# Performance work log

Hardware: AMD Instinct MI355X
Metric: run time of the kernel (lower is better)

The kernel has to match this reference:

```python
import jax, jax.numpy as jnp
import numpy as np
import math

N = 128
SIZE = N * N
K = 16
ORDER = 2
DIM = 2

def _exponents(order):
    # 2D Taylor monomial exponents (a,b) with 1 <= a+b <= order
    return [(a, d - a) for d in range(1, order + 1) for a in range(d, -1, -1)]

EXPS = _exponents(ORDER)
NUM_DERIV = len(EXPS)  # n(n+3)/2 = 5 for order 2, matches TP_layer.num_derivatives


def setup_inputs() -> dict:
    key = jax.random.key(0)
    k0, k1, k2, k3, k4 = jax.random.split(key, 5)
    B = 32
    x = jax.random.normal(k0, (B, SIZE), dtype=jnp.float32)
    points = jax.random.uniform(k1, (B, SIZE, DIM), dtype=jnp.float32)
    edge_index = jax.random.randint(k2, (B, SIZE * K), 0, SIZE)
    dist = jax.random.uniform(k3, (B, SIZE, K), dtype=jnp.float32)
    dt = jnp.float32(0.01)
    # PDELinear weight: shape (1, 1, num_derivatives), uniform(-0.1, 0.1)
    weight = jax.random.uniform(k4, (1, 1, NUM_DERIV), dtype=jnp.float32,
                                minval=-0.1, maxval=0.1)
    return {"x": x, "points": points, "edge_index": edge_index,
            "dt": dt, "dist": dist, "weight": weight}


def _solve_derivatives(points, knn_points, values, knn_values, dist):
    # points: [B,S,2]  knn_points: [B,S,K,2]  values: [B,S]  knn_values: [B,S,K]
    off = knn_points - points[:, :, None, :]          # [B,S,K,2]
    dx, dy = off[..., 0], off[..., 1]
    cols = [(dx ** a) * (dy ** b) / (math.factorial(a) * math.factorial(b))
            for (a, b) in EXPS]
    A = jnp.stack(cols, axis=-1)                      # [B,S,K,D] Taylor design matrix
    rhs = knn_values - values[..., None]              # [B,S,K]
    Aw = A * dist[..., None]                          # weighted least squares
    bw = rhs * dist
    AtA = jnp.einsum('bski,bskj->bsij', Aw, Aw)       # [B,S,D,D]
    Atb = jnp.einsum('bski,bsk->bsi', Aw, bw)         # [B,S,D]
    ridge = jnp.float32(1e-6) * jnp.eye(NUM_DERIV, dtype=A.dtype)
    deriv = jnp.linalg.solve(AtA + ridge, Atb[..., None])[..., 0]  # [B,S,D]
    return deriv


def reference(x, points, edge_index, dt, dist, weight):
    B = x.shape[0]
    values = x.reshape(B, SIZE)
    # per-batch kNN gather (vectorized index_select)
    knn_p = jnp.take_along_axis(points, edge_index[..., None], axis=1)
    knn_p = knn_p.reshape(B, SIZE, K, DIM)
    knn_v = jnp.take_along_axis(values[..., None], edge_index[..., None], axis=1)
    knn_v = knn_v.reshape(B, SIZE, K)
    deriv = _solve_derivatives(points, knn_p, values, knn_v, dist)
    deriv = jax.lax.stop_gradient(deriv)              # torch.no_grad in original
    du = jnp.sum(deriv * weight[0], axis=-1)          # PDELinear broadcast + sum -> [B,S]
    return x + dt * du
```

## Files before the change

kernel.cpp:

```cpp
#include <hip/hip_runtime.h>

#define TPL_SIZE 16384
#define TPL_K 16
#define TPL_ND 5
#define TPL_BLK 512
#define TPL_PTS 4
#define TPL_SPAN (TPL_BLK * TPL_PTS)
#define TPL_BPB (TPL_SIZE / TPL_SPAN)
#define TPL_NXCD 8

typedef __attribute__((ext_vector_type(2))) float f32x2;

__global__ __launch_bounds__(TPL_BLK, 2) void tp_lds_kernel(
    const float* __restrict__ x,
    const float* __restrict__ points,
    const int*   __restrict__ edge_index,
    const float* __restrict__ dtp,
    const float* __restrict__ dist,
    const float* __restrict__ weight,
    float* __restrict__ out)
{
    extern __shared__ uint2 lds_pv[];

    const int tid = threadIdx.x;
    const int blk = blockIdx.x;

    const int xcd   = blk & (TPL_NXCD - 1);
    const int batch = xcd * 4 + (blk >> 6);
    const int chunk = (blk >> 3) & (TPL_BPB - 1);

    const size_t base = (size_t)batch * TPL_SIZE + chunk * TPL_SPAN;

    int4   ci[4];
    float4 cw[4];
    {
        const int4*   ei = reinterpret_cast<const int4*>(edge_index + (base + tid) * TPL_K);
        const float4* dw = reinterpret_cast<const float4*>(dist      + (base + tid) * TPL_K);
        ci[0] = ei[0]; ci[1] = ei[1]; ci[2] = ei[2]; ci[3] = ei[3];
        cw[0] = dw[0]; cw[1] = dw[1]; cw[2] = dw[2]; cw[3] = dw[3];
    }

    {
        const float4* pb4 = reinterpret_cast<const float4*>(points + (size_t)batch * TPL_SIZE * 2);
        const float2* xb2 = reinterpret_cast<const float2*>(x + (size_t)batch * TPL_SIZE);
        uint4* lds4 = reinterpret_cast<uint4*>(lds_pv);
        #pragma unroll
        for (int k = 0; k < TPL_SIZE / (2 * TPL_BLK); ++k) {
            int g = k * TPL_BLK + tid;
            float4 pp = pb4[g];
            float2 xv = xb2[g];
            unsigned ux0 = (unsigned)(pp.x * 65536.0f);
            unsigned uy0 = (unsigned)(pp.y * 65536.0f);
            unsigned ux1 = (unsigned)(pp.z * 65536.0f);
            unsigned uy1 = (unsigned)(pp.w * 65536.0f);
            if (ux0 > 65535u) ux0 = 65535u;
            if (uy0 > 65535u) uy0 = 65535u;
            if (ux1 > 65535u) ux1 = 65535u;
            if (uy1 > 65535u) uy1 = 65535u;
            uint4 wv;
            wv.x = ux0 | (uy0 << 16);
            wv.y = __float_as_uint(xv.x);
            wv.z = ux1 | (uy1 << 16);
            wv.w = __float_as_uint(xv.y);
            lds4[g] = wv;
        }
    }
    __syncthreads();

    const float wt0 = weight[0], wt1 = weight[1], wt2 = weight[2],
                wt3 = weight[3], wt4 = weight[4];
    const float dtv = dtp[0];

    #pragma unroll
    for (int p = 0; p < TPL_PTS; ++p) {
        int4   ni[4];
        float4 nw[4];
        if (p < TPL_PTS - 1) {
            const size_t rown = base + (p + 1) * TPL_BLK + tid;
            const int4*   ei = reinterpret_cast<const int4*>(edge_index + rown * TPL_K);
            const float4* dw = reinterpret_cast<const float4*>(dist      + rown * TPL_K);
            ni[0] = ei[0]; ni[1] = ei[1]; ni[2] = ei[2]; ni[3] = ei[3];
            nw[0] = dw[0]; nw[1] = dw[1]; nw[2] = dw[2]; nw[3] = dw[3];
        }

        const int    s   = chunk * TPL_SPAN + p * TPL_BLK + tid;
        const size_t row = base + p * TPL_BLK + tid;

        uint2 se = lds_pv[s];
        unsigned sx = se.x & 0xffffu;
        unsigned sy = se.x >> 16;
        float    sv = __uint_as_float(se.y);

        int ids[TPL_K] = {ci[0].x, ci[0].y, ci[0].z, ci[0].w,
                          ci[1].x, ci[1].y, ci[1].z, ci[1].w,
                          ci[2].x, ci[2].y, ci[2].z, ci[2].w,
                          ci[3].x, ci[3].y, ci[3].z, ci[3].w};
        float wgt[TPL_K] = {cw[0].x, cw[0].y, cw[0].z, cw[0].w,
                            cw[1].x, cw[1].y, cw[1].z, cw[1].w,
                            cw[2].x, cw[2].y, cw[2].z, cw[2].w,
                            cw[3].x, cw[3].y, cw[3].z, cw[3].w};

        uint2 nb[TPL_K];
        #pragma unroll
        for (int t = 0; t < TPL_K; ++t) nb[t] = lds_pv[ids[t] & (TPL_SIZE - 1)];

        f32x2 ata2[15], atb2[TPL_ND];
        #pragma unroll
        for (int i = 0; i < 15; ++i) ata2[i] = (f32x2)0.0f;
        #pragma unroll
        for (int i = 0; i < TPL_ND; ++i) atb2[i] = (f32x2)0.0f;

        #pragma unroll
        for (int tt = 0; tt < TPL_K / 2; ++tt) {
            const int t0 = 2 * tt, t1 = 2 * tt + 1;
            int dxi0 = (int)(nb[t0].x & 0xffffu) - (int)sx;
            int dyi0 = (int)(nb[t0].x >> 16)     - (int)sy;
            int dxi1 = (int)(nb[t1].x & 0xffffu) - (int)sx;
            int dyi1 = (int)(nb[t1].x >> 16)     - (int)sy;
            f32x2 dx = (f32x2){(float)dxi0, (float)dxi1} * 0x1p-16f;
            f32x2 dy = (f32x2){(float)dyi0, (float)dyi1} * 0x1p-16f;
            f32x2 w  = {wgt[t0], wgt[t1]};
            f32x2 nv = {__uint_as_float(nb[t0].y), __uint_as_float(nb[t1].y)};
            f32x2 hw = w * 0.5f;
            f32x2 a[TPL_ND];
            a[0] = dx * w;
            a[1] = dy * w;
            a[2] = dx * dx * hw;
            a[3] = dx * dy * w;
            a[4] = dy * dy * hw;
            f32x2 bwv = (nv - sv) * w;
            int c = 0;
            #pragma unroll
            for (int i = 0; i < TPL_ND; ++i) {
                #pragma unroll
                for (int j = i; j < TPL_ND; ++j) { ata2[c] += a[i] * a[j]; ++c; }
                atb2[i] += a[i] * bwv;
            }
        }

        float ata[15], atb[TPL_ND];
        #pragma unroll
        for (int i = 0; i < 15; ++i) ata[i] = ata2[i].x + ata2[i].y;
        #pragma unroll
        for (int i = 0; i < TPL_ND; ++i) atb[i] = atb2[i].x + atb2[i].y;

        float M[TPL_ND][TPL_ND], r[TPL_ND], pinv[TPL_ND];
        {
            int c = 0;
            #pragma unroll
            for (int i = 0; i < TPL_ND; ++i) {
                #pragma unroll
                for (int j = i; j < TPL_ND; ++j) { M[i][j] = ata[c]; M[j][i] = ata[c]; ++c; }
                r[i] = atb[i];
                M[i][i] += 1e-6f;
            }
        }
        #pragma unroll
        for (int i = 0; i < TPL_ND; ++i) {
            float inv = __builtin_amdgcn_rcpf(M[i][i]);
            pinv[i] = inv;
            #pragma unroll
            for (int j = i + 1; j < TPL_ND; ++j) {
                float f = M[j][i] * inv;
                #pragma unroll
                for (int cc = i + 1; cc < TPL_ND; ++cc) M[j][cc] -= f * M[i][cc];
                r[j] -= f * r[i];
            }
        }
        float sol[TPL_ND];
        #pragma unroll
        for (int i = TPL_ND - 1; i >= 0; --i) {
            float sv2 = r[i];
            #pragma unroll
            for (int cc = i + 1; cc < TPL_ND; ++cc) sv2 -= M[i][cc] * sol[cc];
            sol[i] = sv2 * pinv[i];
        }

        float du = sol[0] * wt0 + sol[1] * wt1 + sol[2] * wt2
                 + sol[3] * wt3 + sol[4] * wt4;
        out[row] = sv + dtv * du;

        if (p < TPL_PTS - 1) {
            #pragma unroll
            for (int q = 0; q < 4; ++q) { ci[q] = ni[q]; cw[q] = nw[q]; }
        }
    }
}

extern "C" void kernel_launch(void* const* d_in, const int* in_sizes, int n_in,
                              void* d_out, int out_size, void* d_ws, size_t ws_size,
                              hipStream_t stream) {
    const float* x          = (const float*)d_in[0];
    const float* points     = (const float*)d_in[1];
    const int*   edge_index = (const int*)d_in[2];
    const float* dtp        = (const float*)d_in[3];
    const float* dist       = (const float*)d_in[4];
    const float* weight     = (const float*)d_in[5];
    float* out = (float*)d_out;

    int total = out_size;
    int grid  = total / TPL_SPAN;
    size_t lds_bytes = (size_t)TPL_SIZE * sizeof(uint2);

    tp_lds_kernel<<<grid, TPL_BLK, lds_bytes, stream>>>(
        x, points, edge_index, dtp, dist, weight, out);
}
```

Measured before the change: 21.04 us.

## Process two points per thread in packed f32x2 lanes including the solve

Each thread now handles two points at a time (A and B) packed into the two lanes of f32x2 vectors. Accumulation, Gaussian elimination and back-substitution all run on packed math, so the scalar 5x5 solve is vectorized. Previously only the 16-neighbor accumulation was split across lanes, followed by a horizontal reduction. Prefetching now loads the next pair's indices and weights, which doubles register pressure for the index and weight buffers and risks lower occupancy at 512 threads with 2 blocks.

```diff
diff --git a/kernel.cpp b/kernel.cpp
--- a/kernel.cpp
+++ b/kernel.cpp
@@ -5,6 +5,7 @@
 #define TPL_ND 5
 #define TPL_BLK 512
 #define TPL_PTS 4
+#define TPL_PAIRS (TPL_PTS / 2)
 #define TPL_SPAN (TPL_BLK * TPL_PTS)
 #define TPL_BPB (TPL_SIZE / TPL_SPAN)
 #define TPL_NXCD 8
@@ -31,13 +32,18 @@
 
     const size_t base = (size_t)batch * TPL_SIZE + chunk * TPL_SPAN;
 
-    int4   ci[4];
-    float4 cw[4];
+    int4   ciA[4], ciB[4];
+    float4 cwA[4], cwB[4];
     {
-        const int4*   ei = reinterpret_cast<const int4*>(edge_index + (base + tid) * TPL_K);
-        const float4* dw = reinterpret_cast<const float4*>(dist      + (base + tid) * TPL_K);
-        ci[0] = ei[0]; ci[1] = ei[1]; ci[2] = ei[2]; ci[3] = ei[3];
-        cw[0] = dw[0]; cw[1] = dw[1]; cw[2] = dw[2]; cw[3] = dw[3];
+        const int4*   eA = reinterpret_cast<const int4*>(edge_index + (base + tid) * TPL_K);
+        const float4* dA = reinterpret_cast<const float4*>(dist      + (base + tid) * TPL_K);
+        const int4*   eB = reinterpret_cast<const int4*>(edge_index + (base + TPL_BLK + tid) * TPL_K);
+        const float4* dB = reinterpret_cast<const float4*>(dist      + (base + TPL_BLK + tid) * TPL_K);
+        #pragma unroll
+        for (int q = 0; q < 4; ++q) {
+            ciA[q] = eA[q]; cwA[q] = dA[q];
+            ciB[q] = eB[q]; cwB[q] = dB[q];
+        }
     }
 
     {
@@ -72,37 +78,54 @@
     const float dtv = dtp[0];
 
     #pragma unroll
-    for (int p = 0; p < TPL_PTS; ++p) {
-        int4   ni[4];
-        float4 nw[4];
-        if (p < TPL_PTS - 1) {
-            const size_t rown = base + (p + 1) * TPL_BLK + tid;
-            const int4*   ei = reinterpret_cast<const int4*>(edge_index + rown * TPL_K);
-            const float4* dw = reinterpret_cast<const float4*>(dist      + rown * TPL_K);
-            ni[0] = ei[0]; ni[1] = ei[1]; ni[2] = ei[2]; ni[3] = ei[3];
-            nw[0] = dw[0]; nw[1] = dw[1]; nw[2] = dw[2]; nw[3] = dw[3];
-        }
-
-        const int    s   = chunk * TPL_SPAN + p * TPL_BLK + tid;
-        const size_t row = base + p * TPL_BLK + tid;
-
-        uint2 se = lds_pv[s];
-        unsigned sx = se.x & 0xffffu;
-        unsigned sy = se.x >> 16;
-        float    sv = __uint_as_float(se.y);
-
-        int ids[TPL_K] = {ci[0].x, ci[0].y, ci[0].z, ci[0].w,
-                          ci[1].x, ci[1].y, ci[1].z, ci[1].w,
-                          ci[2].x, ci[2].y, ci[2].z, ci[2].w,
-                          ci[3].x, ci[3].y, ci[3].z, ci[3].w};
-        float wgt[TPL_K] = {cw[0].x, cw[0].y, cw[0].z, cw[0].w,
-                            cw[1].x, cw[1].y, cw[1].z, cw[1].w,
-                            cw[2].x, cw[2].y, cw[2].z, cw[2].w,
-                            cw[3].x, cw[3].y, cw[3].z, cw[3].w};
-
-        uint2 nb[TPL_K];
-        #pragma unroll
-        for (int t = 0; t < TPL_K; ++t) nb[t] = lds_pv[ids[t] & (TPL_SIZE - 1)];
+    for (int pp = 0; pp < TPL_PAIRS; ++pp) {
+        const int    sA   = chunk * TPL_SPAN + (2 * pp) * TPL_BLK + tid;
+        const int    sB   = sA + TPL_BLK;
+        const size_t rowA = base + (2 * pp) * TPL_BLK + tid;
+        const size_t rowB = rowA + TPL_BLK;
+
+        uint2 seA = lds_pv[sA];
+        uint2 seB = lds_pv[sB];
+        const int sxA = (int)(seA.x & 0xffffu), syA = (int)(seA.x >> 16);
+        const int sxB = (int)(seB.x & 0xffffu), syB = (int)(seB.x >> 16);
+        const f32x2 sv2 = {__uint_as_float(seA.y), __uint_as_float(seB.y)};
+
+        int   idsA[TPL_K], idsB[TPL_K];
+        f32x2 wgt2[TPL_K];
+        #pragma unroll
+        for (int q = 0; q < 4; ++q) {
+            idsA[4*q+0] = ciA[q].x; idsA[4*q+1] = ciA[q].y;
+            idsA[4*q+2] = ciA[q].z; idsA[4*q+3] = ciA[q].w;
+            idsB[4*q+0] = ciB[q].x; idsB[4*q+1] = ciB[q].y;
+            idsB[4*q+2] = ciB[q].z; idsB[4*q+3] = ciB[q].w;
+            wgt2[4*q+0] = (f32x2){cwA[q].x, cwB[q].x};
+            wgt2[4*q+1] = (f32x2){cwA[q].y, cwB[q].y};
+            wgt2[4*q+2] = (f32x2){cwA[q].z, cwB[q].z};
+            wgt2[4*q+3] = (f32x2){cwA[q].w, cwB[q].w};
+        }
+
+        uint2 nA[TPL_K], nB[TPL_K];
+        #pragma unroll
+        for (int t = 0; t < TPL_K; ++t) {
+            nA[t] = lds_pv[idsA[t] & (TPL_SIZE - 1)];
+            nB[t] = lds_pv[idsB[t] & (TPL_SIZE - 1)];
+        }
+
+        int4   niA[4], niB[4];
+        float4 nwA[4], nwB[4];
+        if (pp + 1 < TPL_PAIRS) {
+            const size_t rA = base + (2 * (pp + 1)) * TPL_BLK + tid;
+            const size_t rB = rA + TPL_BLK;
+            const int4*   eA = reinterpret_cast<const int4*>(edge_index + rA * TPL_K);
+            const float4* dA = reinterpret_cast<const float4*>(dist      + rA * TPL_K);
+            const int4*   eB = reinterpret_cast<const int4*>(edge_index + rB * TPL_K);
+            const float4* dB = reinterpret_cast<const float4*>(dist      + rB * TPL_K);
+            #pragma unroll
+            for (int q = 0; q < 4; ++q) {
+                niA[q] = eA[q]; nwA[q] = dA[q];
+                niB[q] = eB[q]; nwB[q] = dB[q];
+            }
+        }
 
         f32x2 ata2[15], atb2[TPL_ND];
         #pragma unroll
@@ -111,16 +134,15 @@
         for (int i = 0; i < TPL_ND; ++i) atb2[i] = (f32x2)0.0f;
 
         #pragma unroll
-        for (int tt = 0; tt < TPL_K / 2; ++tt) {
-            const int t0 = 2 * tt, t1 = 2 * tt + 1;
-            int dxi0 = (int)(nb[t0].x & 0xffffu) - (int)sx;
-            int dyi0 = (int)(nb[t0].x >> 16)     - (int)sy;
-            int dxi1 = (int)(nb[t1].x & 0xffffu) - (int)sx;
-            int dyi1 = (int)(nb[t1].x >> 16)     - (int)sy;
-            f32x2 dx = (f32x2){(float)dxi0, (float)dxi1} * 0x1p-16f;
-            f32x2 dy = (f32x2){(float)dyi0, (float)dyi1} * 0x1p-16f;
-            f32x2 w  = {wgt[t0], wgt[t1]};
-            f32x2 nv = {__uint_as_float(nb[t0].y), __uint_as_float(nb[t1].y)};
+        for (int t = 0; t < TPL_K; ++t) {
+            int dxiA = (int)(nA[t].x & 0xffffu) - sxA;
+            int dyiA = (int)(nA[t].x >> 16)     - syA;
+            int dxiB = (int)(nB[t].x & 0xffffu) - sxB;
+            int dyiB = (int)(nB[t].x >> 16)     - syB;
+            f32x2 dx = (f32x2){(float)dxiA, (float)dxiB} * 0x1p-16f;
+            f32x2 dy = (f32x2){(float)dyiA, (float)dyiB} * 0x1p-16f;
+            f32x2 w  = wgt2[t];
+            f32x2 nv = {__uint_as_float(nA[t].y), __uint_as_float(nB[t].y)};
             f32x2 hw = w * 0.5f;
             f32x2 a[TPL_ND];
             a[0] = dx * w;
@@ -128,7 +150,7 @@
             a[2] = dx * dx * hw;
             a[3] = dx * dy * w;
             a[4] = dy * dy * hw;
-            f32x2 bwv = (nv - sv) * w;
+            f32x2 bwv = (nv - sv2) * w;
             int c = 0;
             #pragma unroll
             for (int i = 0; i < TPL_ND; ++i) {
@@ -138,51 +160,50 @@
             }
         }
 
-        float ata[15], atb[TPL_ND];
-        #pragma unroll
-        for (int i = 0; i < 15; ++i) ata[i] = ata2[i].x + ata2[i].y;
-        #pragma unroll
-        for (int i = 0; i < TPL_ND; ++i) atb[i] = atb2[i].x + atb2[i].y;
-
-        float M[TPL_ND][TPL_ND], r[TPL_ND], pinv[TPL_ND];
+        f32x2 M2[TPL_ND][TPL_ND], r2[TPL_ND], pinv2[TPL_ND];
         {
             int c = 0;
             #pragma unroll
             for (int i = 0; i < TPL_ND; ++i) {
                 #pragma unroll
-                for (int j = i; j < TPL_ND; ++j) { M[i][j] = ata[c]; M[j][i] = ata[c]; ++c; }
-                r[i] = atb[i];
-                M[i][i] += 1e-6f;
+                for (int j = i; j < TPL_ND; ++j) { M2[i][j] = ata2[c]; M2[j][i] = ata2[c]; ++c; }
+                r2[i] = atb2[i];
+                M2[i][i] += 1e-6f;
             }
         }
         #pragma unroll
         for (int i = 0; i < TPL_ND; ++i) {
-            float inv = __builtin_amdgcn_rcpf(M[i][i]);
-            pinv[i] = inv;
+            f32x2 inv2 = {__builtin_amdgcn_rcpf(M2[i][i].x),
+                          __builtin_amdgcn_rcpf(M2[i][i].y)};
+            pinv2[i] = inv2;
             #pragma unroll
             for (int j = i + 1; j < TPL_ND; ++j) {
-                float f = M[j][i] * inv;
+                f32x2 f = M2[j][i] * inv2;
                 #pragma unroll
-                for (int cc = i + 1; cc < TPL_ND; ++cc) M[j][cc] -= f * M[i][cc];
-                r[j] -= f * r[i];
-            }
-        }
-        float sol[TPL_ND];
+                for (int cc = i + 1; cc < TPL_ND; ++cc) M2[j][cc] -= f * M2[i][cc];
+                r2[j] -= f * r2[i];
+            }
+        }
+        f32x2 sol2[TPL_ND];
         #pragma unroll
         for (int i = TPL_ND - 1; i >= 0; --i) {
-            float sv2 = r[i];
-            #pragma unroll
-            for (int cc = i + 1; cc < TPL_ND; ++cc) sv2 -= M[i][cc] * sol[cc];
-            sol[i] = sv2 * pinv[i];
-        }
-
-        float du = sol[0] * wt0 + sol[1] * wt1 + sol[2] * wt2
-                 + sol[3] * wt3 + sol[4] * wt4;
-        out[row] = sv + dtv * du;
-
-        if (p < TPL_PTS - 1) {
-            #pragma unroll
-            for (int q = 0; q < 4; ++q) { ci[q] = ni[q]; cw[q] = nw[q]; }
+            f32x2 acc = r2[i];
+            #pragma unroll
+            for (int cc = i + 1; cc < TPL_ND; ++cc) acc -= M2[i][cc] * sol2[cc];
+            sol2[i] = acc * pinv2[i];
+        }
+
+        f32x2 du2 = sol2[0] * wt0 + sol2[1] * wt1 + sol2[2] * wt2
+                  + sol2[3] * wt3 + sol2[4] * wt4;
+        out[rowA] = sv2.x + dtv * du2.x;
+        out[rowB] = sv2.y + dtv * du2.y;
+
+        if (pp + 1 < TPL_PAIRS) {
+            #pragma unroll
+            for (int q = 0; q < 4; ++q) {
+                ciA[q] = niA[q]; cwA[q] = nwA[q];
+                ciB[q] = niB[q]; cwB[q] = nwB[q];
+            }
         }
     }
 }
```

After: 21.67 us. +3.0%, slower.

## Pre-pack point/value table in separate kernel and bulk-load it into LDS

Applied to the files above, without the earlier changes.

Adds a pack kernel that quantizes points and interleaves them with x into a uint2 table in workspace. The main kernel then fills LDS with direct global-to-LDS loads instead of having each block repeat the conversion. The next row's index/weight prefetch moves to after the neighbor gathers, and the index mask is dropped. The cost is an extra launch plus a table write and read round-trip. Blocks of the same batch no longer redo the packing work, though they still each load the full table.

```diff
diff --git a/kernel.cpp b/kernel.cpp
--- a/kernel.cpp
+++ b/kernel.cpp
@@ -11,7 +11,182 @@
 
 typedef __attribute__((ext_vector_type(2))) float f32x2;
 
+__global__ __launch_bounds__(256) void tp_pack_kernel(
+    const float* __restrict__ x,
+    const float* __restrict__ points,
+    uint2* __restrict__ table,
+    int total)
+{
+    int gid = blockIdx.x * blockDim.x + threadIdx.x;
+    if (gid >= total) return;
+    float2 p = reinterpret_cast<const float2*>(points)[gid];
+    float  v = x[gid];
+    unsigned ux = (unsigned)(p.x * 65536.0f);
+    unsigned uy = (unsigned)(p.y * 65536.0f);
+    if (ux > 65535u) ux = 65535u;
+    if (uy > 65535u) uy = 65535u;
+    uint2 e;
+    e.x = ux | (uy << 16);
+    e.y = __float_as_uint(v);
+    table[gid] = e;
+}
+
 __global__ __launch_bounds__(TPL_BLK, 2) void tp_lds_kernel(
+    const uint2* __restrict__ table,
+    const int*   __restrict__ edge_index,
+    const float* __restrict__ dtp,
+    const float* __restrict__ dist,
+    const float* __restrict__ weight,
+    float* __restrict__ out)
+{
+    extern __shared__ uint2 lds_pv[];
+
+    const int tid = threadIdx.x;
+    const int blk = blockIdx.x;
+
+    const int xcd   = blk & (TPL_NXCD - 1);
+    const int batch = xcd * 4 + (blk >> 6);
+    const int chunk = (blk >> 3) & (TPL_BPB - 1);
+
+    const size_t base = (size_t)batch * TPL_SIZE + chunk * TPL_SPAN;
+
+    int4   ci[4];
+    float4 cw[4];
+    {
+        const int4*   ei = reinterpret_cast<const int4*>(edge_index + (base + tid) * TPL_K);
+        const float4* dw = reinterpret_cast<const float4*>(dist      + (base + tid) * TPL_K);
+        ci[0] = ei[0]; ci[1] = ei[1]; ci[2] = ei[2]; ci[3] = ei[3];
+        cw[0] = dw[0]; cw[1] = dw[1]; cw[2] = dw[2]; cw[3] = dw[3];
+    }
+
+    {
+        const uint32_t* tb = reinterpret_cast<const uint32_t*>(table + (size_t)batch * TPL_SIZE);
+        uint32_t* lraw = reinterpret_cast<uint32_t*>(lds_pv);
+        #pragma unroll
+        for (int k = 0; k < (TPL_SIZE * 8) / (TPL_BLK * 16); ++k) {
+            int i = k * TPL_BLK + tid;
+            __builtin_amdgcn_global_load_lds(
+                (const __attribute__((address_space(1))) uint32_t*)(tb) + (size_t)i * 4,
+                (__attribute__((address_space(3))) uint32_t*)(lraw) + (size_t)i * 4,
+                16, 0, 0);
+        }
+    }
+    __syncthreads();
+
+    const float wt0 = weight[0], wt1 = weight[1], wt2 = weight[2],
+                wt3 = weight[3], wt4 = weight[4];
+    const float dtv = dtp[0];
+
+    #pragma unroll
+    for (int p = 0; p < TPL_PTS; ++p) {
+        const int    s   = chunk * TPL_SPAN + p * TPL_BLK + tid;
+        const size_t row = base + p * TPL_BLK + tid;
+
+        uint2 se = lds_pv[s];
+        const int sx = (int)(se.x & 0xffffu);
+        const int sy = (int)(se.x >> 16);
+        const float sv = __uint_as_float(se.y);
+
+        int ids[TPL_K] = {ci[0].x, ci[0].y, ci[0].z, ci[0].w,
+                          ci[1].x, ci[1].y, ci[1].z, ci[1].w,
+                          ci[2].x, ci[2].y, ci[2].z, ci[2].w,
+                          ci[3].x, ci[3].y, ci[3].z, ci[3].w};
+        float wgt[TPL_K] = {cw[0].x, cw[0].y, cw[0].z, cw[0].w,
+                            cw[1].x, cw[1].y, cw[1].z, cw[1].w,
+                            cw[2].x, cw[2].y, cw[2].z, cw[2].w,
+                            cw[3].x, cw[3].y, cw[3].z, cw[3].w};
+
+        uint2 nb[TPL_K];
+        #pragma unroll
+        for (int t = 0; t < TPL_K; ++t) nb[t] = lds_pv[ids[t]];
+
+        if (p < TPL_PTS - 1) {
+            const size_t rown = base + (p + 1) * TPL_BLK + tid;
+            const int4*   ei = reinterpret_cast<const int4*>(edge_index + rown * TPL_K);
+            const float4* dw = reinterpret_cast<const float4*>(dist      + rown * TPL_K);
+            #pragma unroll
+            for (int q = 0; q < 4; ++q) { ci[q] = ei[q]; cw[q] = dw[q]; }
+        }
+
+        f32x2 ata2[15], atb2[TPL_ND];
+        #pragma unroll
+        for (int i = 0; i < 15; ++i) ata2[i] = (f32x2)0.0f;
+        #pragma unroll
+        for (int i = 0; i < TPL_ND; ++i) atb2[i] = (f32x2)0.0f;
+
+        #pragma unroll
+        for (int tt = 0; tt < TPL_K / 2; ++tt) {
+            const int t0 = 2 * tt, t1 = 2 * tt + 1;
+            int dxi0 = (int)(nb[t0].x & 0xffffu) - sx;
+            int dyi0 = (int)(nb[t0].x >> 16)     - sy;
+            int dxi1 = (int)(nb[t1].x & 0xffffu) - sx;
+            int dyi1 = (int)(nb[t1].x >> 16)     - sy;
+            f32x2 dx = (f32x2){(float)dxi0, (float)dxi1} * 0x1p-16f;
+            f32x2 dy = (f32x2){(float)dyi0, (float)dyi1} * 0x1p-16f;
+            f32x2 w  = {wgt[t0], wgt[t1]};
+            f32x2 nv = {__uint_as_float(nb[t0].y), __uint_as_float(nb[t1].y)};
+            f32x2 hw = w * 0.5f;
+            f32x2 a[TPL_ND];
+            a[0] = dx * w;
+            a[1] = dy * w;
+            a[2] = dx * dx * hw;
+            a[3] = dx * dy * w;
+            a[4] = dy * dy * hw;
+            f32x2 bwv = (nv - sv) * w;
+            int c = 0;
+            #pragma unroll
+            for (int i = 0; i < TPL_ND; ++i) {
+                #pragma unroll
+                for (int j = i; j < TPL_ND; ++j) { ata2[c] += a[i] * a[j]; ++c; }
+                atb2[i] += a[i] * bwv;
+            }
+        }
+
+        float ata[15], atb[TPL_ND];
+        #pragma unroll
+        for (int i = 0; i < 15; ++i) ata[i] = ata2[i].x + ata2[i].y;
+        #pragma unroll
+        for (int i = 0; i < TPL_ND; ++i) atb[i] = atb2[i].x + atb2[i].y;
+
+        float M[TPL_ND][TPL_ND], r[TPL_ND], pinv[TPL_ND];
+        {
+            int c = 0;
+            #pragma unroll
+            for (int i = 0; i < TPL_ND; ++i) {
+                #pragma unroll
+                for (int j = i; j < TPL_ND; ++j) { M[i][j] = ata[c]; M[j][i] = ata[c]; ++c; }
+                r[i] = atb[i];
+                M[i][i] += 1e-6f;
+            }
+        }
+        #pragma unroll
+        for (int i = 0; i < TPL_ND; ++i) {
+            float inv = __builtin_amdgcn_rcpf(M[i][i]);
+            pinv[i] = inv;
+            #pragma unroll
+            for (int j = i + 1; j < TPL_ND; ++j) {
+                float f = M[j][i] * inv;
+                #pragma unroll
+                for (int cc = i + 1; cc < TPL_ND; ++cc) M[j][cc] -= f * M[i][cc];
+                r[j] -= f * r[i];
+            }
+        }
+        float sol[TPL_ND];
+        #pragma unroll
+        for (int i = TPL_ND - 1; i >= 0; --i) {
+            float sv2 = r[i];
+            #pragma unroll
+            for (int cc = i + 1; cc < TPL_ND; ++cc) sv2 -= M[i][cc] * sol[cc];
+            sol[i] = sv2 * pinv[i];
+        }
+
+        float du = sol[0] * wt0 + sol[1] * wt1 + sol[2] * wt2
+                 + sol[3] * wt3 + sol[4] * wt4;
+        out[row] = sv + dtv * du;
+    }
+}
+
+__global__ __launch_bounds__(TPL_BLK, 2) void tp_lds_fallback_kernel(
     const float* __restrict__ x,
     const float* __restrict__ points,
     const int*   __restrict__ edge_index,
@@ -21,25 +196,20 @@
     float* __restrict__ out)
 {
     extern __shared__ uint2 lds_pv[];
-
     const int tid = threadIdx.x;
     const int blk = blockIdx.x;
-
     const int xcd   = blk & (TPL_NXCD - 1);
     const int batch = xcd * 4 + (blk >> 6);
     const int chunk = (blk >> 3) & (TPL_BPB - 1);
-
     const size_t base = (size_t)batch * TPL_SIZE + chunk * TPL_SPAN;
 
-    int4   ci[4];
-    float4 cw[4];
+    int4 ci[4]; float4 cw[4];
     {
         const int4*   ei = reinterpret_cast<const int4*>(edge_index + (base + tid) * TPL_K);
         const float4* dw = reinterpret_cast<const float4*>(dist      + (base + tid) * TPL_K);
         ci[0] = ei[0]; ci[1] = ei[1]; ci[2] = ei[2]; ci[3] = ei[3];
         cw[0] = dw[0]; cw[1] = dw[1]; cw[2] = dw[2]; cw[3] = dw[3];
     }
-
     {
         const float4* pb4 = reinterpret_cast<const float4*>(points + (size_t)batch * TPL_SIZE * 2);
         const float2* xb2 = reinterpret_cast<const float2*>(x + (size_t)batch * TPL_SIZE);
@@ -58,10 +228,8 @@
             if (ux1 > 65535u) ux1 = 65535u;
             if (uy1 > 65535u) uy1 = 65535u;
             uint4 wv;
-            wv.x = ux0 | (uy0 << 16);
-            wv.y = __float_as_uint(xv.x);
-            wv.z = ux1 | (uy1 << 16);
-            wv.w = __float_as_uint(xv.y);
+            wv.x = ux0 | (uy0 << 16); wv.y = __float_as_uint(xv.x);
+            wv.z = ux1 | (uy1 << 16); wv.w = __float_as_uint(xv.y);
             lds4[g] = wv;
         }
     }
@@ -73,24 +241,12 @@
 
     #pragma unroll
     for (int p = 0; p < TPL_PTS; ++p) {
-        int4   ni[4];
-        float4 nw[4];
-        if (p < TPL_PTS - 1) {
-            const size_t rown = base + (p + 1) * TPL_BLK + tid;
-            const int4*   ei = reinterpret_cast<const int4*>(edge_index + rown * TPL_K);
-            const float4* dw = reinterpret_cast<const float4*>(dist      + rown * TPL_K);
-            ni[0] = ei[0]; ni[1] = ei[1]; ni[2] = ei[2]; ni[3] = ei[3];
-            nw[0] = dw[0]; nw[1] = dw[1]; nw[2] = dw[2]; nw[3] = dw[3];
-        }
-
         const int    s   = chunk * TPL_SPAN + p * TPL_BLK + tid;
         const size_t row = base + p * TPL_BLK + tid;
-
         uint2 se = lds_pv[s];
-        unsigned sx = se.x & 0xffffu;
-        unsigned sy = se.x >> 16;
-        float    sv = __uint_as_float(se.y);
-
+        const int sx = (int)(se.x & 0xffffu);
+        const int sy = (int)(se.x >> 16);
+        const float sv = __uint_as_float(se.y);
         int ids[TPL_K] = {ci[0].x, ci[0].y, ci[0].z, ci[0].w,
                           ci[1].x, ci[1].y, ci[1].z, ci[1].w,
                           ci[2].x, ci[2].y, ci[2].z, ci[2].w,
@@ -99,51 +255,41 @@
                             cw[1].x, cw[1].y, cw[1].z, cw[1].w,
                             cw[2].x, cw[2].y, cw[2].z, cw[2].w,
                             cw[3].x, cw[3].y, cw[3].z, cw[3].w};
-
         uint2 nb[TPL_K];
         #pragma unroll
-        for (int t = 0; t < TPL_K; ++t) nb[t] = lds_pv[ids[t] & (TPL_SIZE - 1)];
-
-        f32x2 ata2[15], atb2[TPL_ND];
-        #pragma unroll
-        for (int i = 0; i < 15; ++i) ata2[i] = (f32x2)0.0f;
-        #pragma unroll
-        for (int i = 0; i < TPL_ND; ++i) atb2[i] = (f32x2)0.0f;
-
-        #pragma unroll
-        for (int tt = 0; tt < TPL_K / 2; ++tt) {
-            const int t0 = 2 * tt, t1 = 2 * tt + 1;
-            int dxi0 = (int)(nb[t0].x & 0xffffu) - (int)sx;
-            int dyi0 = (int)(nb[t0].x >> 16)     - (int)sy;
-            int dxi1 = (int)(nb[t1].x & 0xffffu) - (int)sx;
-            int dyi1 = (int)(nb[t1].x >> 16)     - (int)sy;
-            f32x2 dx = (f32x2){(float)dxi0, (float)dxi1} * 0x1p-16f;
-            f32x2 dy = (f32x2){(float)dyi0, (float)dyi1} * 0x1p-16f;
-            f32x2 w  = {wgt[t0], wgt[t1]};
-            f32x2 nv = {__uint_as_float(nb[t0].y), __uint_as_float(nb[t1].y)};
-            f32x2 hw = w * 0.5f;
-            f32x2 a[TPL_ND];
-            a[0] = dx * w;
-            a[1] = dy * w;
-            a[2] = dx * dx * hw;
-            a[3] = dx * dy * w;
-            a[4] = dy * dy * hw;
-            f32x2 bwv = (nv - sv) * w;
+        for (int t = 0; t < TPL_K; ++t) nb[t] = lds_pv[ids[t]];
+        if (p < TPL_PTS - 1) {
+            const size_t rown = base + (p + 1) * TPL_BLK + tid;
+            const int4*   ei = reinterpret_cast<const int4*>(edge_index + rown * TPL_K);
+            const float4* dw = reinterpret_cast<const float4*>(dist      + rown * TPL_K);
+            #pragma unroll
+            for (int q = 0; q < 4; ++q) { ci[q] = ei[q]; cw[q] = dw[q]; }
+        }
+        float ata[15], atb[TPL_ND];
+        #pragma unroll
+        for (int i = 0; i < 15; ++i) ata[i] = 0.0f;
+        #pragma unroll
+        for (int i = 0; i < TPL_ND; ++i) atb[i] = 0.0f;
+        #pragma unroll
+        for (int t = 0; t < TPL_K; ++t) {
+            float w = wgt[t];
+            int dxi = (int)(nb[t].x & 0xffffu) - sx;
+            int dyi = (int)(nb[t].x >> 16)     - sy;
+            float dx = (float)dxi * 0x1p-16f;
+            float dy = (float)dyi * 0x1p-16f;
+            float nv = __uint_as_float(nb[t].y);
+            float a[TPL_ND];
+            a[0] = dx * w; a[1] = dy * w;
+            a[2] = 0.5f * dx * dx * w; a[3] = dx * dy * w; a[4] = 0.5f * dy * dy * w;
+            float bwv = (nv - sv) * w;
             int c = 0;
             #pragma unroll
             for (int i = 0; i < TPL_ND; ++i) {
                 #pragma unroll
-                for (int j = i; j < TPL_ND; ++j) { ata2[c] += a[i] * a[j]; ++c; }
-                atb2[i] += a[i] * bwv;
-            }
-        }
-
-        float ata[15], atb[TPL_ND];
-        #pragma unroll
-        for (int i = 0; i < 15; ++i) ata[i] = ata2[i].x + ata2[i].y;
-        #pragma unroll
-        for (int i = 0; i < TPL_ND; ++i) atb[i] = atb2[i].x + atb2[i].y;
-
+                for (int j = i; j < TPL_ND; ++j) ata[c++] += a[i] * a[j];
+                atb[i] += a[i] * bwv;
+            }
+        }
         float M[TPL_ND][TPL_ND], r[TPL_ND], pinv[TPL_ND];
         {
             int c = 0;
@@ -175,15 +321,9 @@
             for (int cc = i + 1; cc < TPL_ND; ++cc) sv2 -= M[i][cc] * sol[cc];
             sol[i] = sv2 * pinv[i];
         }
-
         float du = sol[0] * wt0 + sol[1] * wt1 + sol[2] * wt2
                  + sol[3] * wt3 + sol[4] * wt4;
         out[row] = sv + dtv * du;
-
-        if (p < TPL_PTS - 1) {
-            #pragma unroll
-            for (int q = 0; q < 4; ++q) { ci[q] = ni[q]; cw[q] = nw[q]; }
-        }
     }
 }
 
@@ -202,6 +342,14 @@
     int grid  = total / TPL_SPAN;
     size_t lds_bytes = (size_t)TPL_SIZE * sizeof(uint2);
 
-    tp_lds_kernel<<<grid, TPL_BLK, lds_bytes, stream>>>(
-        x, points, edge_index, dtp, dist, weight, out);
+    size_t need = (size_t)total * sizeof(uint2);
+    if (ws_size >= need) {
+        uint2* table = (uint2*)d_ws;
+        tp_pack_kernel<<<(total + 255) / 256, 256, 0, stream>>>(x, points, table, total);
+        tp_lds_kernel<<<grid, TPL_BLK, lds_bytes, stream>>>(
+            table, edge_index, dtp, dist, weight, out);
+    } else {
+        tp_lds_fallback_kernel<<<grid, TPL_BLK, lds_bytes, stream>>>(
+            x, points, edge_index, dtp, dist, weight, out);
+    }
 }
```

Measured after the change: 25.27 us. 20.1% more time.
